# Kernel optimization log

Measured on AMD Instinct MI355X. Metric: run time of the kernel, lower is better.

## Reference

```python
import jax, jax.numpy as jnp
import numpy as np
from jax import lax

N, C, T, H, W = 2, 128, 8, 56, 56
NH, DK, DV, DD = 1, 16, 128, 16
D_HID = NH * DK + DV  # 144
KS = (3, 7, 7)
PAD = [(1, 1), (3, 3), (3, 3)]  # 'same' padding for (3,7,7)
EPS = 1e-6


def _l2norm(x, axis):
    # matches module: x / sqrt(sum(x^2) + eps)
    return x / jnp.sqrt(jnp.sum(x * x, axis=axis, keepdims=True) + EPS)


def setup_inputs() -> dict:
    key = jax.random.key(0)
    k1, k2, k3 = jax.random.split(key, 3)
    x = jax.random.normal(k1, (N, C, T, H, W), dtype=jnp.float32)
    W_proj = jax.random.normal(k2, (D_HID, C), dtype=jnp.float32) * (1.0 / np.sqrt(C))
    W_H2 = jax.random.normal(k3, (DD, 1) + KS, dtype=jnp.float32) * (1.0 / np.sqrt(float(np.prod(KS))))
    return {"x": x, "W_proj": W_proj, "W_H2": W_H2}


def reference(x, W_proj, W_H2):
    b, c, t, h, w = x.shape
    # 1x1x1 projection conv == per-pixel channel matmul
    xp = jnp.einsum('bcthw,oc->bothw', x, W_proj)  # (b, 144, t, h, w)
    q = xp[:, :NH * DK]  # (b, nh*dk, t, h, w)
    v = xp[:, NH * DK:]  # (b, dv,    t, h, w)
    # normalization (kernel_type 'V': kernel = q directly)
    q = _l2norm(q.reshape(b, NH, DK, t, h, w), axis=2)  # L2 over dk
    v = _l2norm(v, axis=1)                              # L2 over channels
    # H2: each v channel treated as its own 1-channel sample -> dd feature maps
    v_ = v.reshape(b * DV, 1, t, h, w)
    V = lax.conv_general_dilated(
        v_, W_H2, window_strides=(1, 1, 1), padding=PAD,
        dimension_numbers=('NCDHW', 'OIDHW', 'NCDHW'))  # (b*dv, dd, t, h, w)
    feat = V.reshape(b, DV, DD, t, h, w)
    # per-pixel tiny matmul: out[.., v, n] = sum_k q[.., n, k] * feat[.., v, k]  (dk == dd)
    out = jnp.einsum('bnkthw,bvkthw->bvnthw', q, feat)
    # rearrange '(b t h w) nh v -> b (nh v) t h w' with einsum output (a, dv, nh)
    return out.reshape(b, DV * NH, t, h, w)
```

## Files before the change

kernel.cpp:

```cpp
#include <hip/hip_runtime.h>
#include <hip/hip_bf16.h>

constexpr int NB   = 2;
constexpr int CIN  = 128;
constexpr int TT   = 8;
constexpr int HH   = 56;
constexpr int WW   = 56;
constexpr int S    = TT * HH * WW;
constexpr int DK   = 16;
constexpr int DV   = 128;
constexpr int TAPS = 147;
constexpr int NOUT = DK + DV;
constexpr int VPT = 10, VPH = 62, VPWA = 64;
constexpr int PLANE_A = VPT * VPH * VPWA;
constexpr int BSTR = 72;
constexpr float EPSf = 1e-6f;

typedef short bf16x8 __attribute__((ext_vector_type(8)));
typedef float f32x4  __attribute__((ext_vector_type(4)));

static __device__ __forceinline__ short f2bf(float f) {
    __hip_bfloat16 h = __float2bfloat16(f);
    short s;
    __builtin_memcpy(&s, &h, 2);
    return s;
}

__global__ __launch_bounds__(256) void k_twp(
    const float* __restrict__ Wp, short* __restrict__ Wpfrag)
{
    int gid = blockIdx.x * 256 + threadIdx.x;
    if (gid >= 9 * 4 * 64) return;
    int lane = gid & 63;
    int kb   = (gid >> 6) & 3;
    int mt   = gid >> 8;
    int n = mt * 16 + (lane & 15);
    int c0 = kb * 32 + (lane >> 4) * 8;
#pragma unroll
    for (int j = 0; j < 8; ++j)
        Wpfrag[(size_t)gid * 8 + j] = f2bf(Wp[n * CIN + c0 + j]);
}

__global__ __launch_bounds__(256) void k_proj(
    const float* __restrict__ x, const short* __restrict__ Wpfrag,
    float* __restrict__ qn, short* __restrict__ vclb)
{
    int tid  = threadIdx.x;
    int lane = tid & 63;
    int wv   = tid >> 6;
    int bid  = blockIdx.x;
    int b    = bid / (S / 128);
    int pbas = (bid - b * (S / 128)) * 128 + wv * 32;

    const float* xb = x + (size_t)b * CIN * S;
    int col = lane & 15;
    int g   = lane >> 4;

    bf16x8 bx[2][4];
#pragma unroll
    for (int n2 = 0; n2 < 2; ++n2) {
        int p = pbas + n2 * 16 + col;
#pragma unroll
        for (int kb = 0; kb < 4; ++kb) {
            const float* xs = xb + (size_t)(kb * 32 + g * 8) * S + p;
#pragma unroll
            for (int j = 0; j < 8; ++j)
                bx[n2][kb][j] = f2bf(xs[(size_t)j * S]);
        }
    }

    f32x4 acc[9][2];
#pragma unroll
    for (int mt = 0; mt < 9; ++mt) {
        acc[mt][0] = {0.f, 0.f, 0.f, 0.f};
        acc[mt][1] = {0.f, 0.f, 0.f, 0.f};
    }

    const bf16x8* wf = reinterpret_cast<const bf16x8*>(Wpfrag);
#pragma unroll
    for (int mt = 0; mt < 9; ++mt) {
#pragma unroll
        for (int kb = 0; kb < 4; ++kb) {
            bf16x8 aw = wf[(mt * 4 + kb) * 64 + lane];
            acc[mt][0] = __builtin_amdgcn_mfma_f32_16x16x32_bf16(
                aw, bx[0][kb], acc[mt][0], 0, 0, 0);
            acc[mt][1] = __builtin_amdgcn_mfma_f32_16x16x32_bf16(
                aw, bx[1][kb], acc[mt][1], 0, 0, 0);
        }
    }

#pragma unroll
    for (int n2 = 0; n2 < 2; ++n2) {
        float ssq = 0.f, ssv = 0.f;
#pragma unroll
        for (int r = 0; r < 4; ++r) ssq += acc[0][n2][r] * acc[0][n2][r];
#pragma unroll
        for (int mt = 1; mt < 9; ++mt)
#pragma unroll
            for (int r = 0; r < 4; ++r) ssv += acc[mt][n2][r] * acc[mt][n2][r];
        ssq += __shfl_xor(ssq, 16, 64);
        ssq += __shfl_xor(ssq, 32, 64);
        ssv += __shfl_xor(ssv, 16, 64);
        ssv += __shfl_xor(ssv, 32, 64);
        float qsc = 1.0f / sqrtf(ssq + EPSf);
        float vsc = 1.0f / sqrtf(ssv + EPSf);

        int p = pbas + n2 * 16 + col;
#pragma unroll
        for (int r = 0; r < 4; ++r)
            qn[((size_t)b * DK + (4 * g + r)) * S + p] = acc[0][n2][r] * qsc;

        int t  = p / (HH * WW);
        int hw = p - t * (HH * WW);
        int h  = hw / WW;
        int w  = hw - h * WW;
        size_t pp = (size_t)(t + 1) * (VPH * VPWA) + (size_t)(h + 3) * VPWA + (w + 3);
        short* vb = vclb + (size_t)b * 128 * PLANE_A + pp;
#pragma unroll
        for (int mt = 1; mt < 9; ++mt)
#pragma unroll
            for (int r = 0; r < 4; ++r) {
                int c = (mt - 1) * 16 + 4 * g + r;
                vb[(size_t)c * PLANE_A] = f2bf(acc[mt][n2][r] * vsc);
            }
    }
}

__global__ __launch_bounds__(256) void k_out(
    const short* __restrict__ vclb, const float* __restrict__ qn,
    const float* __restrict__ wh2, float* __restrict__ out)
{
    __shared__ short weff_b[56 * 168];
    __shared__ char  upool[2 * 64 * BSTR * 2];

    int tid  = threadIdx.x;
    int lane = tid & 63;
    int wv   = tid >> 6;
    int bid = blockIdx.x;
    int nid = (bid & 7) * 112 + (bid >> 3);
    int b   = nid / 448;
    int rem = nid - b * 448;
    int t   = rem / 56, h = rem - t * 56;
    int pbase = t * (HH * WW) + h * WW;

    float* q_s = reinterpret_cast<float*>(upool);
    for (int i = tid; i < DK * WW; i += 256) {
        int k = i / 56, w = i - k * 56;
        q_s[i] = qn[((size_t)b * DK + k) * S + pbase + w];
    }
    __syncthreads();

    if (tid < 224) {
        int w = tid % 56, q4 = tid / 56;
        float qr[DK];
#pragma unroll
        for (int k = 0; k < DK; ++k) qr[k] = q_s[k * 56 + w];
#pragma unroll 1
        for (int tap = q4; tap < TAPS; tap += 4) {
            float a = 0.f;
#pragma unroll
            for (int k = 0; k < DK; ++k)
                a = fmaf(qr[k], wh2[k * TAPS + tap], a);
            int row = tap / 7, d = tap - row * 7;
            weff_b[w * 168 + row * 8 + d] = f2bf(a);
        }
    }
    __syncthreads();

    short* band = reinterpret_cast<short*>(upool);
    {
        int* bi = reinterpret_cast<int*>(band);
        for (int i = tid; i < 2 * 64 * BSTR / 2; i += 256) bi[i] = 0;
    }
    __syncthreads();

    int e1 = tid;
    int w1 = e1 / 7, d1 = e1 - w1 * 7;
    int e2 = tid + 256;
    int w2 = e2 / 7, d2 = e2 - w2 * 7;
    bool has2 = (e2 < 392);
    bool has1 = (e1 < 392);

    if (has1) band[w1 * BSTR + w1 + d1] = weff_b[w1 * 168 + d1];
    if (has2) band[w2 * BSTR + w2 + d2] = weff_b[w2 * 168 + d2];
    __syncthreads();

    int col = lane & 15, g = lane >> 4;
    int cbase = wv * 32;

    f32x4 acc[2][4];
#pragma unroll
    for (int m2 = 0; m2 < 2; ++m2)
#pragma unroll
        for (int n = 0; n < 4; ++n) acc[m2][n] = {0.f, 0.f, 0.f, 0.f};

    const short* vb = vclb + (size_t)b * 128 * PLANE_A;

#pragma unroll 1
    for (int r = 0; r < 21; ++r) {
        const short* cur = band + (r & 1) * (64 * BSTR);
        int dz = r / 7, dy = r - dz * 7;
        size_t rowo = (size_t)(t + dz) * (VPH * VPWA) + (size_t)(h + dy) * VPWA;

        bf16x8 av[2][2];
#pragma unroll
        for (int m2 = 0; m2 < 2; ++m2) {
            const short* ap = vb + (size_t)(cbase + m2 * 16 + col) * PLANE_A
                                 + rowo + g * 8;
            av[m2][0] = *reinterpret_cast<const bf16x8*>(ap);
            av[m2][1] = *reinterpret_cast<const bf16x8*>(ap + 32);
        }
        bf16x8 bbf[4][2];
#pragma unroll
        for (int n = 0; n < 4; ++n) {
            const short* bp = cur + (n * 16 + col) * BSTR + g * 8;
            bbf[n][0] = *reinterpret_cast<const bf16x8*>(bp);
            bbf[n][1] = *reinterpret_cast<const bf16x8*>(bp + 32);
        }
#pragma unroll
        for (int n = 0; n < 4; ++n) {
            acc[0][n] = __builtin_amdgcn_mfma_f32_16x16x32_bf16(
                av[0][0], bbf[n][0], acc[0][n], 0, 0, 0);
            acc[0][n] = __builtin_amdgcn_mfma_f32_16x16x32_bf16(
                av[0][1], bbf[n][1], acc[0][n], 0, 0, 0);
            acc[1][n] = __builtin_amdgcn_mfma_f32_16x16x32_bf16(
                av[1][0], bbf[n][0], acc[1][n], 0, 0, 0);
            acc[1][n] = __builtin_amdgcn_mfma_f32_16x16x32_bf16(
                av[1][1], bbf[n][1], acc[1][n], 0, 0, 0);
        }

        if (r < 20) {
            short* nxt = band + ((r + 1) & 1) * (64 * BSTR);
            int ro = (r + 1) * 8;
            if (has1) nxt[w1 * BSTR + w1 + d1] = weff_b[w1 * 168 + ro + d1];
            if (has2) nxt[w2 * BSTR + w2 + d2] = weff_b[w2 * 168 + ro + d2];
        }
        __syncthreads();
    }

#pragma unroll
    for (int m2 = 0; m2 < 2; ++m2) {
#pragma unroll
        for (int n = 0; n < 4; ++n) {
            int w = n * 16 + col;
            if (w < 56) {
                size_t ob = ((size_t)b * DV + cbase + m2 * 16 + 4 * g) * S + pbase + w;
#pragma unroll
                for (int rr = 0; rr < 4; ++rr)
                    out[ob + (size_t)rr * S] = acc[m2][n][rr];
            }
        }
    }
}

extern "C" void kernel_launch(void* const* d_in, const int* in_sizes, int n_in,
                              void* d_out, int out_size, void* d_ws, size_t ws_size,
                              hipStream_t stream)
{
    const float* x   = (const float*)d_in[0];
    const float* Wp  = (const float*)d_in[1];
    const float* wh2 = (const float*)d_in[2];
    float* out = (float*)d_out;

    float* ws     = (float*)d_ws;
    short* Wpfrag = (short*)ws;
    float* qn     = ws + 9216;
    short* vclb   = (short*)(qn + (size_t)NB * DK * S);

    size_t vclb_bytes = (size_t)NB * 128 * PLANE_A * sizeof(short);

    k_twp <<<dim3(9), dim3(256), 0, stream>>>(Wp, Wpfrag);
    hipMemsetAsync(vclb, 0, vclb_bytes, stream);
    k_proj<<<dim3(NB * S / 128), dim3(256), 0, stream>>>(x, Wpfrag, qn, vclb);
    k_out <<<dim3(NB * TT * HH), dim3(256), 0, stream>>>(vclb, qn, wh2, out);
}
```

Before: 115.2 us.

## Prefetch next-row V operands, skip zero band MFMAs, pad band stride

```diff
diff --git a/kernel.cpp b/kernel.cpp
--- a/kernel.cpp
+++ b/kernel.cpp
@@ -13,7 +13,7 @@
 constexpr int NOUT = DK + DV;
 constexpr int VPT = 10, VPH = 62, VPWA = 64;
 constexpr int PLANE_A = VPT * VPH * VPWA;
-constexpr int BSTR = 72;
+constexpr int BSTR = 74;
 constexpr float EPSf = 1e-6f;
 
 typedef short bf16x8 __attribute__((ext_vector_type(8)));
@@ -126,7 +126,7 @@
     }
 }
 
-__global__ __launch_bounds__(256) void k_out(
+__global__ __launch_bounds__(256, 2) void k_out(
     const short* __restrict__ vclb, const float* __restrict__ qn,
     const float* __restrict__ wh2, float* __restrict__ out)
 {
@@ -143,6 +143,19 @@
     int t   = rem / 56, h = rem - t * 56;
     int pbase = t * (HH * WW) + h * WW;
 
+    int col = lane & 15, g = lane >> 4;
+    int cbase = wv * 32;
+
+    const short* vb  = vclb + (size_t)b * 128 * PLANE_A;
+    const short* ap0 = vb + (size_t)(cbase + col) * PLANE_A + g * 8;
+    const short* ap1 = vb + (size_t)(cbase + 16 + col) * PLANE_A + g * 8;
+    size_t o0 = (size_t)(t + 0) * (VPH * VPWA) + (size_t)(h + 0) * VPWA;
+    bf16x8 avc[2][2], avn[2][2];
+    avc[0][0] = *reinterpret_cast<const bf16x8*>(ap0 + o0);
+    avc[0][1] = *reinterpret_cast<const bf16x8*>(ap0 + o0 + 32);
+    avc[1][0] = *reinterpret_cast<const bf16x8*>(ap1 + o0);
+    avc[1][1] = *reinterpret_cast<const bf16x8*>(ap1 + o0 + 32);
+
     float* q_s = reinterpret_cast<float*>(upool);
     for (int i = tid; i < DK * WW; i += 256) {
         int k = i / 56, w = i - k * 56;
@@ -179,63 +192,63 @@
     int e2 = tid + 256;
     int w2 = e2 / 7, d2 = e2 - w2 * 7;
     bool has2 = (e2 < 392);
-    bool has1 = (e1 < 392);
-
-    if (has1) band[w1 * BSTR + w1 + d1] = weff_b[w1 * 168 + d1];
+
+    band[w1 * BSTR + w1 + d1] = weff_b[w1 * 168 + d1];
     if (has2) band[w2 * BSTR + w2 + d2] = weff_b[w2 * 168 + d2];
     __syncthreads();
 
-    int col = lane & 15, g = lane >> 4;
-    int cbase = wv * 32;
-
     f32x4 acc[2][4];
 #pragma unroll
     for (int m2 = 0; m2 < 2; ++m2)
 #pragma unroll
         for (int n = 0; n < 4; ++n) acc[m2][n] = {0.f, 0.f, 0.f, 0.f};
-
-    const short* vb = vclb + (size_t)b * 128 * PLANE_A;
 
 #pragma unroll 1
     for (int r = 0; r < 21; ++r) {
+        if (r < 20) {
+            int r1 = r + 1;
+            int dz = r1 / 7, dy = r1 - dz * 7;
+            size_t o = (size_t)(t + dz) * (VPH * VPWA) + (size_t)(h + dy) * VPWA;
+            avn[0][0] = *reinterpret_cast<const bf16x8*>(ap0 + o);
+            avn[0][1] = *reinterpret_cast<const bf16x8*>(ap0 + o + 32);
+            avn[1][0] = *reinterpret_cast<const bf16x8*>(ap1 + o);
+            avn[1][1] = *reinterpret_cast<const bf16x8*>(ap1 + o + 32);
+        }
+
         const short* cur = band + (r & 1) * (64 * BSTR);
-        int dz = r / 7, dy = r - dz * 7;
-        size_t rowo = (size_t)(t + dz) * (VPH * VPWA) + (size_t)(h + dy) * VPWA;
-
-        bf16x8 av[2][2];
+        bf16x8 b00 = *reinterpret_cast<const bf16x8*>(cur + (0 * 16 + col) * BSTR + g * 8);
+        bf16x8 b10 = *reinterpret_cast<const bf16x8*>(cur + (1 * 16 + col) * BSTR + g * 8);
+        bf16x8 b11 = *reinterpret_cast<const bf16x8*>(cur + (1 * 16 + col) * BSTR + 32 + g * 8);
+        bf16x8 b21 = *reinterpret_cast<const bf16x8*>(cur + (2 * 16 + col) * BSTR + 32 + g * 8);
+        bf16x8 b31 = *reinterpret_cast<const bf16x8*>(cur + (3 * 16 + col) * BSTR + 32 + g * 8);
+
 #pragma unroll
         for (int m2 = 0; m2 < 2; ++m2) {
-            const short* ap = vb + (size_t)(cbase + m2 * 16 + col) * PLANE_A
-                                 + rowo + g * 8;
-            av[m2][0] = *reinterpret_cast<const bf16x8*>(ap);
-            av[m2][1] = *reinterpret_cast<const bf16x8*>(ap + 32);
-        }
-        bf16x8 bbf[4][2];
-#pragma unroll
-        for (int n = 0; n < 4; ++n) {
-            const short* bp = cur + (n * 16 + col) * BSTR + g * 8;
-            bbf[n][0] = *reinterpret_cast<const bf16x8*>(bp);
-            bbf[n][1] = *reinterpret_cast<const bf16x8*>(bp + 32);
-        }
-#pragma unroll
-        for (int n = 0; n < 4; ++n) {
-            acc[0][n] = __builtin_amdgcn_mfma_f32_16x16x32_bf16(
-                av[0][0], bbf[n][0], acc[0][n], 0, 0, 0);
-            acc[0][n] = __builtin_amdgcn_mfma_f32_16x16x32_bf16(
-                av[0][1], bbf[n][1], acc[0][n], 0, 0, 0);
-            acc[1][n] = __builtin_amdgcn_mfma_f32_16x16x32_bf16(
-                av[1][0], bbf[n][0], acc[1][n], 0, 0, 0);
-            acc[1][n] = __builtin_amdgcn_mfma_f32_16x16x32_bf16(
-                av[1][1], bbf[n][1], acc[1][n], 0, 0, 0);
+            acc[m2][0] = __builtin_amdgcn_mfma_f32_16x16x32_bf16(
+                avc[m2][0], b00, acc[m2][0], 0, 0, 0);
+            acc[m2][1] = __builtin_amdgcn_mfma_f32_16x16x32_bf16(
+                avc[m2][0], b10, acc[m2][1], 0, 0, 0);
+            acc[m2][1] = __builtin_amdgcn_mfma_f32_16x16x32_bf16(
+                avc[m2][1], b11, acc[m2][1], 0, 0, 0);
+            acc[m2][2] = __builtin_amdgcn_mfma_f32_16x16x32_bf16(
+                avc[m2][1], b21, acc[m2][2], 0, 0, 0);
+            acc[m2][3] = __builtin_amdgcn_mfma_f32_16x16x32_bf16(
+                avc[m2][1], b31, acc[m2][3], 0, 0, 0);
         }
 
         if (r < 20) {
             short* nxt = band + ((r + 1) & 1) * (64 * BSTR);
             int ro = (r + 1) * 8;
-            if (has1) nxt[w1 * BSTR + w1 + d1] = weff_b[w1 * 168 + ro + d1];
+            nxt[w1 * BSTR + w1 + d1] = weff_b[w1 * 168 + ro + d1];
             if (has2) nxt[w2 * BSTR + w2 + d2] = weff_b[w2 * 168 + ro + d2];
         }
         __syncthreads();
+
+#pragma unroll
+        for (int m2 = 0; m2 < 2; ++m2) {
+            avc[m2][0] = avn[m2][0];
+            avc[m2][1] = avn[m2][1];
+        }
     }
 
 #pragma unroll
```

Measured after the change: 123.7 us. +7.4%, slower.

## Skip zero band MFMA blocks and read weights from a padded per-column LDS table

Applied to the files above, without the earlier changes.

```diff
diff --git a/kernel.cpp b/kernel.cpp
--- a/kernel.cpp
+++ b/kernel.cpp
@@ -13,7 +13,8 @@
 constexpr int NOUT = DK + DV;
 constexpr int VPT = 10, VPH = 62, VPWA = 64;
 constexpr int PLANE_A = VPT * VPH * VPWA;
-constexpr int BSTR = 72;
+constexpr int WROW = 22;
+constexpr int WSTRIDE = 21 * WROW;
 constexpr float EPSf = 1e-6f;
 
 typedef short bf16x8 __attribute__((ext_vector_type(8)));
@@ -130,8 +131,8 @@
     const short* __restrict__ vclb, const float* __restrict__ qn,
     const float* __restrict__ wh2, float* __restrict__ out)
 {
-    __shared__ short weff_b[56 * 168];
-    __shared__ char  upool[2 * 64 * BSTR * 2];
+    __shared__ float q_s[DK * WW];
+    __shared__ short wext[56 * WSTRIDE];
 
     int tid  = threadIdx.x;
     int lane = tid & 63;
@@ -143,99 +144,86 @@
     int t   = rem / 56, h = rem - t * 56;
     int pbase = t * (HH * WW) + h * WW;
 
-    float* q_s = reinterpret_cast<float*>(upool);
     for (int i = tid; i < DK * WW; i += 256) {
         int k = i / 56, w = i - k * 56;
         q_s[i] = qn[((size_t)b * DK + k) * S + pbase + w];
     }
+    {
+        int* wz = reinterpret_cast<int*>(wext);
+        for (int i = tid; i < 56 * WSTRIDE / 2; i += 256) wz[i] = 0;
+    }
     __syncthreads();
 
-    if (tid < 224) {
-        int w = tid % 56, q4 = tid / 56;
-        float qr[DK];
-#pragma unroll
-        for (int k = 0; k < DK; ++k) qr[k] = q_s[k * 56 + w];
-#pragma unroll 1
-        for (int tap = q4; tap < TAPS; tap += 4) {
-            float a = 0.f;
-#pragma unroll
-            for (int k = 0; k < DK; ++k)
-                a = fmaf(qr[k], wh2[k * TAPS + tap], a);
-            int row = tap / 7, d = tap - row * 7;
-            weff_b[w * 168 + row * 8 + d] = f2bf(a);
-        }
-    }
-    __syncthreads();
-
-    short* band = reinterpret_cast<short*>(upool);
-    {
-        int* bi = reinterpret_cast<int*>(band);
-        for (int i = tid; i < 2 * 64 * BSTR / 2; i += 256) bi[i] = 0;
-    }
-    __syncthreads();
-
-    int e1 = tid;
-    int w1 = e1 / 7, d1 = e1 - w1 * 7;
-    int e2 = tid + 256;
-    int w2 = e2 / 7, d2 = e2 - w2 * 7;
-    bool has2 = (e2 < 392);
-    bool has1 = (e1 < 392);
-
-    if (has1) band[w1 * BSTR + w1 + d1] = weff_b[w1 * 168 + d1];
-    if (has2) band[w2 * BSTR + w2 + d2] = weff_b[w2 * 168 + d2];
+    for (int e = tid; e < 56 * TAPS; e += 256) {
+        int w = e / TAPS, r = e - w * TAPS;
+        float a = 0.f;
+#pragma unroll
+        for (int k = 0; k < DK; ++k)
+            a = fmaf(q_s[k * 56 + w], wh2[k * TAPS + r], a);
+        int row = r / 7, d = r - row * 7;
+        wext[w * WSTRIDE + row * WROW + d + 8 + (w & 1)] = f2bf(a);
+    }
     __syncthreads();
 
     int col = lane & 15, g = lane >> 4;
     int cbase = wv * 32;
 
+    int boff[5];
+    {
+        const int NN[5] = {0, 1, 1, 2, 3};
+        const int KB[5] = {0, 0, 1, 1, 1};
+#pragma unroll
+        for (int p = 0; p < 5; ++p) {
+            int wl = NN[p] * 16 + col;
+            if (wl > 55) wl = 55;
+            int base = KB[p] * 32 + g * 8 - wl;
+            bool ov = (base >= -7) && (base <= 6);
+            int r0 = ov ? (base + 8 + (wl & 1)) : 0;
+            boff[p] = (wl * WSTRIDE + r0) * 2;
+        }
+    }
+
+    const short* vb0 = vclb + (size_t)b * 128 * PLANE_A
+                     + (size_t)(cbase + col) * PLANE_A + g * 8;
+    const short* vb1 = vb0 + (size_t)16 * PLANE_A;
+
     f32x4 acc[2][4];
 #pragma unroll
     for (int m2 = 0; m2 < 2; ++m2)
 #pragma unroll
         for (int n = 0; n < 4; ++n) acc[m2][n] = {0.f, 0.f, 0.f, 0.f};
 
-    const short* vb = vclb + (size_t)b * 128 * PLANE_A;
-
-#pragma unroll 1
+    const char* wbase = reinterpret_cast<const char*>(wext);
+
+#pragma unroll 3
     for (int r = 0; r < 21; ++r) {
-        const short* cur = band + (r & 1) * (64 * BSTR);
         int dz = r / 7, dy = r - dz * 7;
-        size_t rowo = (size_t)(t + dz) * (VPH * VPWA) + (size_t)(h + dy) * VPWA;
-
-        bf16x8 av[2][2];
-#pragma unroll
-        for (int m2 = 0; m2 < 2; ++m2) {
-            const short* ap = vb + (size_t)(cbase + m2 * 16 + col) * PLANE_A
-                                 + rowo + g * 8;
-            av[m2][0] = *reinterpret_cast<const bf16x8*>(ap);
-            av[m2][1] = *reinterpret_cast<const bf16x8*>(ap + 32);
-        }
-        bf16x8 bbf[4][2];
-#pragma unroll
-        for (int n = 0; n < 4; ++n) {
-            const short* bp = cur + (n * 16 + col) * BSTR + g * 8;
-            bbf[n][0] = *reinterpret_cast<const bf16x8*>(bp);
-            bbf[n][1] = *reinterpret_cast<const bf16x8*>(bp + 32);
-        }
-#pragma unroll
-        for (int n = 0; n < 4; ++n) {
-            acc[0][n] = __builtin_amdgcn_mfma_f32_16x16x32_bf16(
-                av[0][0], bbf[n][0], acc[0][n], 0, 0, 0);
-            acc[0][n] = __builtin_amdgcn_mfma_f32_16x16x32_bf16(
-                av[0][1], bbf[n][1], acc[0][n], 0, 0, 0);
-            acc[1][n] = __builtin_amdgcn_mfma_f32_16x16x32_bf16(
-                av[1][0], bbf[n][0], acc[1][n], 0, 0, 0);
-            acc[1][n] = __builtin_amdgcn_mfma_f32_16x16x32_bf16(
-                av[1][1], bbf[n][1], acc[1][n], 0, 0, 0);
-        }
-
-        if (r < 20) {
-            short* nxt = band + ((r + 1) & 1) * (64 * BSTR);
-            int ro = (r + 1) * 8;
-            if (has1) nxt[w1 * BSTR + w1 + d1] = weff_b[w1 * 168 + ro + d1];
-            if (has2) nxt[w2 * BSTR + w2 + d2] = weff_b[w2 * 168 + ro + d2];
-        }
-        __syncthreads();
+        size_t o = (size_t)(t + dz) * (VPH * VPWA) + (size_t)(h + dy) * VPWA;
+
+        bf16x8 a00 = *reinterpret_cast<const bf16x8*>(vb0 + o);
+        bf16x8 a01 = *reinterpret_cast<const bf16x8*>(vb0 + o + 32);
+        bf16x8 a10 = *reinterpret_cast<const bf16x8*>(vb1 + o);
+        bf16x8 a11 = *reinterpret_cast<const bf16x8*>(vb1 + o + 32);
+
+        int rb = r * (WROW * 2);
+        bf16x8 bb[5];
+#pragma unroll
+        for (int p = 0; p < 5; ++p) {
+            const int* wp = reinterpret_cast<const int*>(wbase + boff[p] + rb);
+            int tmp[4] = {wp[0], wp[1], wp[2], wp[3]};
+            __builtin_memcpy(&bb[p], tmp, 16);
+        }
+
+        acc[0][0] = __builtin_amdgcn_mfma_f32_16x16x32_bf16(a00, bb[0], acc[0][0], 0, 0, 0);
+        acc[0][1] = __builtin_amdgcn_mfma_f32_16x16x32_bf16(a00, bb[1], acc[0][1], 0, 0, 0);
+        acc[0][1] = __builtin_amdgcn_mfma_f32_16x16x32_bf16(a01, bb[2], acc[0][1], 0, 0, 0);
+        acc[0][2] = __builtin_amdgcn_mfma_f32_16x16x32_bf16(a01, bb[3], acc[0][2], 0, 0, 0);
+        acc[0][3] = __builtin_amdgcn_mfma_f32_16x16x32_bf16(a01, bb[4], acc[0][3], 0, 0, 0);
+        acc[1][0] = __builtin_amdgcn_mfma_f32_16x16x32_bf16(a10, bb[0], acc[1][0], 0, 0, 0);
+        acc[1][1] = __builtin_amdgcn_mfma_f32_16x16x32_bf16(a10, bb[1], acc[1][1], 0, 0, 0);
+        acc[1][1] = __builtin_amdgcn_mfma_f32_16x16x32_bf16(a11, bb[2], acc[1][1], 0, 0, 0);
+        acc[1][2] = __builtin_amdgcn_mfma_f32_16x16x32_bf16(a11, bb[3], acc[1][2], 0, 0, 0);
+        acc[1][3] = __builtin_amdgcn_mfma_f32_16x16x32_bf16(a11, bb[4], acc[1][3], 0, 0, 0);
     }
 
 #pragma unroll
```

After: 113.5 us. Within noise of the previous version (-1.5%).
